# Kernel tuning notes

Measured on AMD Instinct MI355X. Metric: run time of the kernel, lower is better.

## Reference

```python
import jax, jax.numpy as jnp
import numpy as np

B, T, D, H = 64, 512, 512, 512


def setup_inputs() -> dict:
    key = jax.random.key(0)
    k1, k2, k3, k4 = jax.random.split(key, 4)
    return {
        "x": jax.random.normal(k1, (B, T, D), dtype=jnp.float32),
        "kernel": jax.random.normal(k2, (D, 4 * H), dtype=jnp.float32) * 0.02,
        "recurrent_kernel": jax.random.normal(k3, (H, 4 * H), dtype=jnp.float32) * 0.02,
        "bias": jax.random.normal(k4, (4 * H,), dtype=jnp.float32) * 0.02,
    }


def reference(x, kernel, recurrent_kernel, bias):
    # Faithful MyLSTM forward, return_sequences=True.
    # tf.split order along last axis: i, f, c, o.
    b = x.shape[0]
    h0 = jnp.zeros((b, H), dtype=x.dtype)
    c0 = jnp.zeros((b, H), dtype=x.dtype)
    xs = jnp.swapaxes(x, 0, 1)  # [T, B, D]

    def step(carry, xt):
        h, c = carry
        # fused gate GEMM; mathematically identical to the 4 separate matmuls
        z = xt @ kernel + h @ recurrent_kernel + bias  # [B, 4H]
        i_t = jax.nn.sigmoid(z[:, 0 * H:1 * H])
        f_t = jax.nn.sigmoid(z[:, 1 * H:2 * H])
        c_tilde = jnp.tanh(z[:, 2 * H:3 * H])
        o_t = jax.nn.sigmoid(z[:, 3 * H:4 * H])
        # NB: module applies tanh to c_t and carries the ACTIVATED cell state
        c_new = jnp.tanh(f_t * c + i_t * c_tilde)
        h_new = o_t * c_new
        return (h_new, c_new), h_new

    (_, _), hs = jax.lax.scan(step, (h0, c0), xs)
    return jnp.swapaxes(hs, 0, 1)  # [B, T, H]
```

## Files before the change

kernel.cpp:

```cpp
#include <hip/hip_runtime.h>
#include <hip/hip_bf16.h>
#include <stdint.h>


#define Bdim 64
#define Tdim 512
#define Ddim 512
#define Hdim 512
#define G4H  2048
#define NG 4
#define NS 32
#define BH (Bdim * Hdim)

typedef __bf16 bf16_t;
typedef __bf16 bf16x8 __attribute__((ext_vector_type(8)));
typedef float  f32x4  __attribute__((ext_vector_type(4)));
typedef uint32_t u32x4 __attribute__((ext_vector_type(4)));
union pv128 { u32x4 u; f32x4 f; bf16x8 h; };
union bu16 { bf16_t b; unsigned short u; };

__device__ __forceinline__ float sigmoid_f(float x) {
  return 1.0f / (1.0f + __expf(-x));
}
__device__ __forceinline__ float tanh_f(float x) {
  return 1.0f - 2.0f / (__expf(2.0f * x) + 1.0f);
}

__global__ void transpose_bf16_512x2048(const float* __restrict__ src,
                                        bf16_t* __restrict__ dst) {
  __shared__ bf16_t tile[64][72];
  int c0 = blockIdx.x * 64;
  int r0 = blockIdx.y * 64;
  int tx = threadIdx.x & 63;
  int ty = threadIdx.x >> 6;
#pragma unroll
  for (int i = 0; i < 64; i += 4)
    tile[ty + i][tx] = (bf16_t)src[(size_t)(r0 + ty + i) * G4H + c0 + tx];
  __syncthreads();
#pragma unroll
  for (int i = 0; i < 64; i += 4)
    dst[(size_t)(c0 + ty + i) * Ddim + r0 + tx] = tile[tx][ty + i];
}

__global__ void cast_bf16(const float* __restrict__ in, bf16_t* __restrict__ out) {
  size_t i = ((size_t)blockIdx.x * blockDim.x + threadIdx.x) * 8;
  f32x4 a = *(const f32x4*)(in + i);
  f32x4 b = *(const f32x4*)(in + i + 4);
  bf16x8 v;
#pragma unroll
  for (int j = 0; j < 4; ++j) { v[j] = (bf16_t)a[j]; v[j + 4] = (bf16_t)b[j]; }
  *(bf16x8*)(out + i) = v;
}

#define MFMA16(A, B, C) __builtin_amdgcn_mfma_f32_16x16x32_bf16(A, B, C, 0, 0, 0)

#define ISSUE_POLL()                                                         \
  asm volatile(                                                              \
      "global_load_dwordx4 %0, %8, off sc0 sc1\n\t"                          \
      "global_load_dwordx4 %1, %8, off offset:16 sc0 sc1\n\t"                \
      "global_load_dwordx4 %2, %8, off offset:128 sc0 sc1\n\t"               \
      "global_load_dwordx4 %3, %8, off offset:144 sc0 sc1\n\t"               \
      "global_load_dwordx4 %4, %8, off offset:256 sc0 sc1\n\t"               \
      "global_load_dwordx4 %5, %8, off offset:272 sc0 sc1\n\t"               \
      "global_load_dwordx4 %6, %8, off offset:384 sc0 sc1\n\t"               \
      "global_load_dwordx4 %7, %8, off offset:400 sc0 sc1"                   \
      : "=v"(p0.f), "=v"(p1.f), "=v"(p2.f), "=v"(p3.f), "=v"(p4.f),          \
        "=v"(p5.f), "=v"(p6.f), "=v"(p7.f)                                   \
      : "v"(hb)                                                              \
      : "memory")

#define CHECK(P)                                                             \
  do {                                                                       \
    bad |= (P.u[0] ^ st) & 15u;                                              \
    bad |= (P.u[1] ^ st) & 15u;                                              \
    bad |= (P.u[2] ^ st) & 15u;                                              \
    bad |= (P.u[3] ^ st) & 15u;                                              \
  } while (0)

#define HU(PA, PB, c)                                                        \
  do {                                                                       \
    pv128 hi_, lo_;                                                          \
    hi_.u[0] = (PA.u[0] >> 16) | (PA.u[1] & 0xFFFF0000u);                    \
    hi_.u[1] = (PA.u[2] >> 16) | (PA.u[3] & 0xFFFF0000u);                    \
    hi_.u[2] = (PB.u[0] >> 16) | (PB.u[1] & 0xFFFF0000u);                    \
    hi_.u[3] = (PB.u[2] >> 16) | (PB.u[3] & 0xFFFF0000u);                    \
    lo_.u[0] = (PA.u[0] & 0xFFF0u) | ((PA.u[1] & 0xFFF0u) << 16);            \
    lo_.u[1] = (PA.u[2] & 0xFFF0u) | ((PA.u[3] & 0xFFF0u) << 16);            \
    lo_.u[2] = (PB.u[0] & 0xFFF0u) | ((PB.u[1] & 0xFFF0u) << 16);            \
    lo_.u[3] = (PB.u[2] & 0xFFF0u) | ((PB.u[3] & 0xFFF0u) << 16);            \
    a0 = MFMA16(hi_.h, Ur[0][c], a0);                                        \
    a1 = MFMA16(hi_.h, Ur[1][c], a1);                                        \
    a2 = MFMA16(hi_.h, Ur[2][c], a2);                                        \
    a3 = MFMA16(hi_.h, Ur[3][c], a3);                                        \
    a0 = MFMA16(lo_.h, Ur[0][c], a0);                                        \
    a1 = MFMA16(lo_.h, Ur[1][c], a1);                                        \
    a2 = MFMA16(lo_.h, Ur[2][c], a2);                                        \
    a3 = MFMA16(lo_.h, Ur[3][c], a3);                                        \
  } while (0)

__launch_bounds__(256, 1)
__global__ void lstm_fused(const bf16_t* __restrict__ xb,
                           const bf16_t* __restrict__ Wt,
                           const bf16_t* __restrict__ Ut,
                           const float* __restrict__ bias,
                           float* __restrict__ out,
                           uint32_t* __restrict__ hbuf) {
  __shared__ float EX[4][4][16][17];

  const int blk  = blockIdx.x;
  const int g    = blk >> 5;
  const int s    = blk & 31;
  const int wv   = threadIdx.x >> 6;
  const int lane = threadIdx.x & 63;
  const int l15  = lane & 15;
  const int l4   = lane >> 4;
  const int b0   = g * 16;
  const int hc0  = s * 16;
  const int k0   = wv * 128;

  bf16x8 Wr[4][4], Ur[4][4];
#pragma unroll
  for (int G = 0; G < 4; ++G) {
    const bf16_t* wsrc = Wt + (size_t)(G * Hdim + hc0 + l15) * Ddim + k0 + l4 * 8;
    const bf16_t* usrc = Ut + (size_t)(G * Hdim + hc0 + l15) * Ddim + k0 + l4 * 8;
#pragma unroll
    for (int c = 0; c < 4; ++c) {
      Wr[G][c] = *(const bf16x8*)(wsrc + c * 32);
      Ur[G][c] = *(const bf16x8*)(usrc + c * 32);
    }
  }

  const int urow = threadIdx.x >> 4;
  const int ucol = threadIdx.x & 15;
  float b4[4];
#pragma unroll
  for (int G = 0; G < 4; ++G) b4[G] = bias[G * Hdim + hc0 + ucol];
  float cstate = 0.f;
  float* outp = out + (size_t)(b0 + urow) * Tdim * Hdim + hc0 + ucol;
  uint32_t* hpub = hbuf + (size_t)(b0 + urow) * Hdim + hc0 + ucol;
  const uint32_t* hrd = hbuf + (size_t)(b0 + l15) * Hdim + k0 + l4 * 8;
  const bf16_t* xrow = xb + (size_t)(b0 + l15) * Tdim * Ddim + l4 * 8 + k0;

  pv128 xr0, xr1, xr2, xr3;
  asm volatile(
      "global_load_dwordx4 %0, %4, off nt\n\t"
      "global_load_dwordx4 %1, %4, off offset:64 nt\n\t"
      "global_load_dwordx4 %2, %4, off offset:128 nt\n\t"
      "global_load_dwordx4 %3, %4, off offset:192 nt\n\t"
      "s_waitcnt vmcnt(0)"
      : "=v"(xr0.f), "=v"(xr1.f), "=v"(xr2.f), "=v"(xr3.f)
      : "v"(xrow) : "memory");
  __builtin_amdgcn_sched_barrier(0);

  bool dead = false;

  for (int t = 0; t < Tdim; ++t) {
    pv128 p0, p1, p2, p3, p4, p5, p6, p7;
    const uint32_t st = (uint32_t)t & 15u;
    const uint32_t* hb = hrd + (((t - 1) & 1) ? BH : 0);

    if (t > 0 && !dead) {
      ISSUE_POLL();
      __builtin_amdgcn_sched_barrier(0);
    }

    f32x4 a0 = {0, 0, 0, 0}, a1 = {0, 0, 0, 0}, a2 = {0, 0, 0, 0}, a3 = {0, 0, 0, 0};
#define XW(c, xv)                                                            \
    a0 = MFMA16(xv.h, Wr[0][c], a0);                                         \
    a1 = MFMA16(xv.h, Wr[1][c], a1);                                         \
    a2 = MFMA16(xv.h, Wr[2][c], a2);                                         \
    a3 = MFMA16(xv.h, Wr[3][c], a3);
    XW(0, xr0) XW(1, xr1) XW(2, xr2) XW(3, xr3)
#undef XW

    if (t > 0) {
      if (!dead) {
        int guard = 0;
        for (;;) {
          asm volatile("s_waitcnt vmcnt(0)" ::: "memory");
          __builtin_amdgcn_sched_barrier(0);
          uint32_t bad = 0;
          CHECK(p0); CHECK(p1); CHECK(p2); CHECK(p3);
          CHECK(p4); CHECK(p5); CHECK(p6); CHECK(p7);
          if (__all(bad == 0)) break;
          if (++guard > 200000) { dead = true; break; }
          ISSUE_POLL();
          __builtin_amdgcn_sched_barrier(0);
        }
      } else {
        p0.u = p1.u = p2.u = p3.u = p4.u = p5.u = p6.u = p7.u = (u32x4)(0u);
      }
      HU(p0, p1, 0);
      HU(p2, p3, 1);
      HU(p4, p5, 2);
      HU(p6, p7, 3);
    }

    {
      const bf16_t* xp = xrow + (size_t)((t + 1 < Tdim) ? t + 1 : Tdim - 1) * Ddim;
      asm volatile(
          "global_load_dwordx4 %0, %4, off nt\n\t"
          "global_load_dwordx4 %1, %4, off offset:64 nt\n\t"
          "global_load_dwordx4 %2, %4, off offset:128 nt\n\t"
          "global_load_dwordx4 %3, %4, off offset:192 nt"
          : "=v"(xr0.f), "=v"(xr1.f), "=v"(xr2.f), "=v"(xr3.f)
          : "v"(xp) : "memory");
    }

#pragma unroll
    for (int G = 0; G < 4; ++G) {
      f32x4 av = (G == 0) ? a0 : (G == 1) ? a1 : (G == 2) ? a2 : a3;
#pragma unroll
      for (int r = 0; r < 4; ++r) EX[wv][G][l4 * 4 + r][l15] = av[r];
    }
    __syncthreads();

    float z0 = EX[0][0][urow][ucol] + EX[1][0][urow][ucol] +
               EX[2][0][urow][ucol] + EX[3][0][urow][ucol] + b4[0];
    float z1 = EX[0][1][urow][ucol] + EX[1][1][urow][ucol] +
               EX[2][1][urow][ucol] + EX[3][1][urow][ucol] + b4[1];
    float z2 = EX[0][2][urow][ucol] + EX[1][2][urow][ucol] +
               EX[2][2][urow][ucol] + EX[3][2][urow][ucol] + b4[2];
    float z3 = EX[0][3][urow][ucol] + EX[1][3][urow][ucol] +
               EX[2][3][urow][ucol] + EX[3][3][urow][ucol] + b4[3];
    float ig = sigmoid_f(z0), fg = sigmoid_f(z1);
    float ct = tanh_f(z2), og = sigmoid_f(z3);
    float cn = tanh_f(fg * cstate + ig * ct);
    cstate = cn;
    float h = og * cn;

    bu16 hh; hh.b = (bf16_t)h;
    bu16 hl; hl.b = (bf16_t)(h - (float)hh.b);
    uint32_t pubw = ((uint32_t)hh.u << 16) | ((uint32_t)hl.u & 0xFFF0u) |
                    ((uint32_t)(t + 1) & 15u);
    uint32_t* dst = hpub + ((t & 1) ? BH : 0);
    asm volatile("global_store_dword %0, %1, off sc0 sc1" ::"v"(dst), "v"(pubw)
                 : "memory");
    __builtin_nontemporal_store(h, outp + (size_t)t * Hdim);

    __syncthreads();

    asm volatile("s_waitcnt vmcnt(0)" ::: "memory");
    __builtin_amdgcn_sched_barrier(0);
  }
}

extern "C" void kernel_launch(void* const* d_in, const int* in_sizes, int n_in,
                              void* d_out, int out_size, void* d_ws, size_t ws_size,
                              hipStream_t stream) {
  const float* x    = (const float*)d_in[0];
  const float* W    = (const float*)d_in[1];
  const float* U    = (const float*)d_in[2];
  const float* bias = (const float*)d_in[3];
  float* out = (float*)d_out;

  unsigned char* ws = (unsigned char*)d_ws;
  uint32_t* hbuf = (uint32_t*)ws;
  bf16_t* Wt = (bf16_t*)(ws + 262144);
  bf16_t* Ut = Wt + (size_t)G4H * Ddim;
  bf16_t* xb = Ut + (size_t)G4H * Ddim;

  hipMemsetAsync(hbuf, 0, 262144, stream);

  cast_bf16<<<(Bdim * Tdim * Ddim) / 2048, 256, 0, stream>>>(x, xb);

  dim3 tgrid(G4H / 64, Ddim / 64);
  transpose_bf16_512x2048<<<tgrid, 256, 0, stream>>>(W, Wt);
  transpose_bf16_512x2048<<<tgrid, 256, 0, stream>>>(U, Ut);

  lstm_fused<<<NG * NS, 256, 0, stream>>>(xb, Wt, Ut, bias, out, hbuf);
}
```

Measured before the change: 1.526 ms.

## Double-buffer LDS exchange, unroll timestep loop, and relax per-step waits

```diff
diff --git a/kernel.cpp b/kernel.cpp
--- a/kernel.cpp
+++ b/kernel.cpp
@@ -69,25 +69,29 @@
       : "v"(hb)                                                              \
       : "memory")
 
-#define CHECK(P)                                                             \
-  do {                                                                       \
-    bad |= (P.u[0] ^ st) & 15u;                                              \
-    bad |= (P.u[1] ^ st) & 15u;                                              \
-    bad |= (P.u[2] ^ st) & 15u;                                              \
-    bad |= (P.u[3] ^ st) & 15u;                                              \
+#define CHECK8()                                                             \
+  do {                                                                       \
+    bad = (p0.u[0] ^ st) & 15u;                                              \
+    bad |= (p1.u[0] ^ st) & 15u;                                             \
+    bad |= (p2.u[0] ^ st) & 15u;                                             \
+    bad |= (p3.u[0] ^ st) & 15u;                                             \
+    bad |= (p4.u[0] ^ st) & 15u;                                             \
+    bad |= (p5.u[0] ^ st) & 15u;                                             \
+    bad |= (p6.u[0] ^ st) & 15u;                                             \
+    bad |= (p7.u[0] ^ st) & 15u;                                             \
   } while (0)
 
 #define HU(PA, PB, c)                                                        \
   do {                                                                       \
     pv128 hi_, lo_;                                                          \
-    hi_.u[0] = (PA.u[0] >> 16) | (PA.u[1] & 0xFFFF0000u);                    \
-    hi_.u[1] = (PA.u[2] >> 16) | (PA.u[3] & 0xFFFF0000u);                    \
-    hi_.u[2] = (PB.u[0] >> 16) | (PB.u[1] & 0xFFFF0000u);                    \
-    hi_.u[3] = (PB.u[2] >> 16) | (PB.u[3] & 0xFFFF0000u);                    \
-    lo_.u[0] = (PA.u[0] & 0xFFF0u) | ((PA.u[1] & 0xFFF0u) << 16);            \
-    lo_.u[1] = (PA.u[2] & 0xFFF0u) | ((PA.u[3] & 0xFFF0u) << 16);            \
-    lo_.u[2] = (PB.u[0] & 0xFFF0u) | ((PB.u[1] & 0xFFF0u) << 16);            \
-    lo_.u[3] = (PB.u[2] & 0xFFF0u) | ((PB.u[3] & 0xFFF0u) << 16);            \
+    hi_.u[0] = __builtin_amdgcn_perm(PA.u[1], PA.u[0], 0x07060302u);         \
+    hi_.u[1] = __builtin_amdgcn_perm(PA.u[3], PA.u[2], 0x07060302u);         \
+    hi_.u[2] = __builtin_amdgcn_perm(PB.u[1], PB.u[0], 0x07060302u);         \
+    hi_.u[3] = __builtin_amdgcn_perm(PB.u[3], PB.u[2], 0x07060302u);         \
+    lo_.u[0] = __builtin_amdgcn_perm(PA.u[1], PA.u[0], 0x05040100u) & 0xFFF0FFF0u; \
+    lo_.u[1] = __builtin_amdgcn_perm(PA.u[3], PA.u[2], 0x05040100u) & 0xFFF0FFF0u; \
+    lo_.u[2] = __builtin_amdgcn_perm(PB.u[1], PB.u[0], 0x05040100u) & 0xFFF0FFF0u; \
+    lo_.u[3] = __builtin_amdgcn_perm(PB.u[3], PB.u[2], 0x05040100u) & 0xFFF0FFF0u; \
     a0 = MFMA16(hi_.h, Ur[0][c], a0);                                        \
     a1 = MFMA16(hi_.h, Ur[1][c], a1);                                        \
     a2 = MFMA16(hi_.h, Ur[2][c], a2);                                        \
@@ -98,6 +102,97 @@
     a3 = MFMA16(lo_.h, Ur[3][c], a3);                                        \
   } while (0)
 
+#define XW(c, xv)                                                            \
+  a0 = MFMA16(xv.h, Wr[0][c], a0);                                           \
+  a1 = MFMA16(xv.h, Wr[1][c], a1);                                           \
+  a2 = MFMA16(xv.h, Wr[2][c], a2);                                           \
+  a3 = MFMA16(xv.h, Wr[3][c], a3);
+
+#define ISSUE_X(X0, X1, X2, X3, ptr)                                         \
+  asm volatile(                                                              \
+      "global_load_dwordx4 %0, %4, off\n\t"                                  \
+      "global_load_dwordx4 %1, %4, off offset:64\n\t"                        \
+      "global_load_dwordx4 %2, %4, off offset:128\n\t"                       \
+      "global_load_dwordx4 %3, %4, off offset:192"                           \
+      : "=v"(X0.f), "=v"(X1.f), "=v"(X2.f), "=v"(X3.f)                       \
+      : "v"(ptr)                                                             \
+      : "memory")
+
+#define EPILOGUE(T, PAR)                                                     \
+  do {                                                                       \
+    _Pragma("unroll")                                                        \
+    for (int G = 0; G < 4; ++G) {                                            \
+      f32x4 av = (G == 0) ? a0 : (G == 1) ? a1 : (G == 2) ? a2 : a3;         \
+      _Pragma("unroll")                                                      \
+      for (int r = 0; r < 4; ++r) EX[PAR][wv][G][l4 * 4 + r][l15] = av[r];   \
+    }                                                                        \
+    __syncthreads();                                                         \
+    float z0 = EX[PAR][0][0][urow][ucol] + EX[PAR][1][0][urow][ucol] +       \
+               EX[PAR][2][0][urow][ucol] + EX[PAR][3][0][urow][ucol] + b4[0];\
+    float z1 = EX[PAR][0][1][urow][ucol] + EX[PAR][1][1][urow][ucol] +       \
+               EX[PAR][2][1][urow][ucol] + EX[PAR][3][1][urow][ucol] + b4[1];\
+    float z2 = EX[PAR][0][2][urow][ucol] + EX[PAR][1][2][urow][ucol] +       \
+               EX[PAR][2][2][urow][ucol] + EX[PAR][3][2][urow][ucol] + b4[2];\
+    float z3 = EX[PAR][0][3][urow][ucol] + EX[PAR][1][3][urow][ucol] +       \
+               EX[PAR][2][3][urow][ucol] + EX[PAR][3][3][urow][ucol] + b4[3];\
+    float ig = sigmoid_f(z0), fg = sigmoid_f(z1);                            \
+    float ct = tanh_f(z2), og = sigmoid_f(z3);                               \
+    float cn = tanh_f(fg * cstate + ig * ct);                                \
+    cstate = cn;                                                             \
+    float h = og * cn;                                                       \
+    bu16 hh; hh.b = (bf16_t)h;                                               \
+    bu16 hl; hl.b = (bf16_t)(h - (float)hh.b);                               \
+    uint32_t pubw = ((uint32_t)hh.u << 16) | ((uint32_t)hl.u & 0xFFF0u) |    \
+                    ((uint32_t)((T) + 1) & 15u);                             \
+    uint32_t* dstp = hpub + ((PAR) ? BH : 0);                                \
+    asm volatile("global_store_dword %0, %1, off sc0 sc1" ::"v"(dstp),       \
+                 "v"(pubw) : "memory");                                      \
+    float* outw = outp + (size_t)(T) * Hdim;                                 \
+    asm volatile("global_store_dword %0, %1, off nt" ::"v"(outw), "v"(h)     \
+                 : "memory");                                                \
+  } while (0)
+
+#define BODY(T, XU0, XU1, XU2, XU3, XL0, XL1, XL2, XL3, PAR)                 \
+  do {                                                                       \
+    const int t_ = (T);                                                      \
+    asm volatile("s_waitcnt vmcnt(2)" ::: "memory");           \
+    __builtin_amdgcn_sched_barrier(0);                                       \
+    const uint32_t st = (uint32_t)t_ & 15u;                                  \
+    const uint32_t* hb = hrd + ((PAR) ? 0 : BH);          \
+    pv128 p0, p1, p2, p3, p4, p5, p6, p7;                                    \
+    ISSUE_POLL();                                                            \
+    {                                                                        \
+      const bf16_t* xp_ =                                                    \
+          xrow + (size_t)((t_ + 1 < Tdim) ? t_ + 1 : Tdim - 1) * Ddim;       \
+      ISSUE_X(XL0, XL1, XL2, XL3, xp_);                                      \
+    }                                                                        \
+    f32x4 a0 = {0, 0, 0, 0}, a1 = {0, 0, 0, 0};                              \
+    f32x4 a2 = {0, 0, 0, 0}, a3 = {0, 0, 0, 0};                              \
+    XW(0, XU0) XW(1, XU1) XW(2, XU2) XW(3, XU3)                              \
+    {                                                                        \
+      uint32_t bad;                                                          \
+      asm volatile("s_waitcnt vmcnt(4)" ::: "memory");       \
+      __builtin_amdgcn_sched_barrier(0);                                     \
+      CHECK8();                                                              \
+      if (!__all(bad == 0)) {                                                \
+        int guard = 0;                                                       \
+        for (;;) {                                                           \
+          ISSUE_POLL();                                                      \
+          asm volatile("s_waitcnt vmcnt(0)" ::: "memory");                   \
+          __builtin_amdgcn_sched_barrier(0);                                 \
+          CHECK8();                                                          \
+          if (__all(bad == 0)) break;                                        \
+          if (++guard > 200000) break;                                       \
+        }                                                                    \
+      }                                                                      \
+    }                                                                        \
+    HU(p0, p1, 0);                                                           \
+    HU(p2, p3, 1);                                                           \
+    HU(p4, p5, 2);                                                           \
+    HU(p6, p7, 3);                                                           \
+    EPILOGUE(t_, PAR);                                                       \
+  } while (0)
+
 __launch_bounds__(256, 1)
 __global__ void lstm_fused(const bf16_t* __restrict__ xb,
                            const bf16_t* __restrict__ Wt,
@@ -105,7 +200,7 @@
                            const float* __restrict__ bias,
                            float* __restrict__ out,
                            uint32_t* __restrict__ hbuf) {
-  __shared__ float EX[4][4][16][17];
+  __shared__ float EX[2][4][4][16][17];
 
   const int blk  = blockIdx.x;
   const int g    = blk >> 5;
@@ -141,108 +236,24 @@
   const uint32_t* hrd = hbuf + (size_t)(b0 + l15) * Hdim + k0 + l4 * 8;
   const bf16_t* xrow = xb + (size_t)(b0 + l15) * Tdim * Ddim + l4 * 8 + k0;
 
-  pv128 xr0, xr1, xr2, xr3;
-  asm volatile(
-      "global_load_dwordx4 %0, %4, off nt\n\t"
-      "global_load_dwordx4 %1, %4, off offset:64 nt\n\t"
-      "global_load_dwordx4 %2, %4, off offset:128 nt\n\t"
-      "global_load_dwordx4 %3, %4, off offset:192 nt\n\t"
-      "s_waitcnt vmcnt(0)"
-      : "=v"(xr0.f), "=v"(xr1.f), "=v"(xr2.f), "=v"(xr3.f)
-      : "v"(xrow) : "memory");
+  pv128 xA0, xA1, xA2, xA3, xB0, xB1, xB2, xB3;
+
+  ISSUE_X(xA0, xA1, xA2, xA3, xrow);
+  asm volatile("s_waitcnt vmcnt(0)" ::: "memory");
   __builtin_amdgcn_sched_barrier(0);
-
-  bool dead = false;
-
-  for (int t = 0; t < Tdim; ++t) {
-    pv128 p0, p1, p2, p3, p4, p5, p6, p7;
-    const uint32_t st = (uint32_t)t & 15u;
-    const uint32_t* hb = hrd + (((t - 1) & 1) ? BH : 0);
-
-    if (t > 0 && !dead) {
-      ISSUE_POLL();
-      __builtin_amdgcn_sched_barrier(0);
-    }
-
-    f32x4 a0 = {0, 0, 0, 0}, a1 = {0, 0, 0, 0}, a2 = {0, 0, 0, 0}, a3 = {0, 0, 0, 0};
-#define XW(c, xv)                                                            \
-    a0 = MFMA16(xv.h, Wr[0][c], a0);                                         \
-    a1 = MFMA16(xv.h, Wr[1][c], a1);                                         \
-    a2 = MFMA16(xv.h, Wr[2][c], a2);                                         \
-    a3 = MFMA16(xv.h, Wr[3][c], a3);
-    XW(0, xr0) XW(1, xr1) XW(2, xr2) XW(3, xr3)
-#undef XW
-
-    if (t > 0) {
-      if (!dead) {
-        int guard = 0;
-        for (;;) {
-          asm volatile("s_waitcnt vmcnt(0)" ::: "memory");
-          __builtin_amdgcn_sched_barrier(0);
-          uint32_t bad = 0;
-          CHECK(p0); CHECK(p1); CHECK(p2); CHECK(p3);
-          CHECK(p4); CHECK(p5); CHECK(p6); CHECK(p7);
-          if (__all(bad == 0)) break;
-          if (++guard > 200000) { dead = true; break; }
-          ISSUE_POLL();
-          __builtin_amdgcn_sched_barrier(0);
-        }
-      } else {
-        p0.u = p1.u = p2.u = p3.u = p4.u = p5.u = p6.u = p7.u = (u32x4)(0u);
-      }
-      HU(p0, p1, 0);
-      HU(p2, p3, 1);
-      HU(p4, p5, 2);
-      HU(p6, p7, 3);
-    }
-
-    {
-      const bf16_t* xp = xrow + (size_t)((t + 1 < Tdim) ? t + 1 : Tdim - 1) * Ddim;
-      asm volatile(
-          "global_load_dwordx4 %0, %4, off nt\n\t"
-          "global_load_dwordx4 %1, %4, off offset:64 nt\n\t"
-          "global_load_dwordx4 %2, %4, off offset:128 nt\n\t"
-          "global_load_dwordx4 %3, %4, off offset:192 nt"
-          : "=v"(xr0.f), "=v"(xr1.f), "=v"(xr2.f), "=v"(xr3.f)
-          : "v"(xp) : "memory");
-    }
-
-#pragma unroll
-    for (int G = 0; G < 4; ++G) {
-      f32x4 av = (G == 0) ? a0 : (G == 1) ? a1 : (G == 2) ? a2 : a3;
-#pragma unroll
-      for (int r = 0; r < 4; ++r) EX[wv][G][l4 * 4 + r][l15] = av[r];
-    }
-    __syncthreads();
-
-    float z0 = EX[0][0][urow][ucol] + EX[1][0][urow][ucol] +
-               EX[2][0][urow][ucol] + EX[3][0][urow][ucol] + b4[0];
-    float z1 = EX[0][1][urow][ucol] + EX[1][1][urow][ucol] +
-               EX[2][1][urow][ucol] + EX[3][1][urow][ucol] + b4[1];
-    float z2 = EX[0][2][urow][ucol] + EX[1][2][urow][ucol] +
-               EX[2][2][urow][ucol] + EX[3][2][urow][ucol] + b4[2];
-    float z3 = EX[0][3][urow][ucol] + EX[1][3][urow][ucol] +
-               EX[2][3][urow][ucol] + EX[3][3][urow][ucol] + b4[3];
-    float ig = sigmoid_f(z0), fg = sigmoid_f(z1);
-    float ct = tanh_f(z2), og = sigmoid_f(z3);
-    float cn = tanh_f(fg * cstate + ig * ct);
-    cstate = cn;
-    float h = og * cn;
-
-    bu16 hh; hh.b = (bf16_t)h;
-    bu16 hl; hl.b = (bf16_t)(h - (float)hh.b);
-    uint32_t pubw = ((uint32_t)hh.u << 16) | ((uint32_t)hl.u & 0xFFF0u) |
-                    ((uint32_t)(t + 1) & 15u);
-    uint32_t* dst = hpub + ((t & 1) ? BH : 0);
-    asm volatile("global_store_dword %0, %1, off sc0 sc1" ::"v"(dst), "v"(pubw)
-                 : "memory");
-    __builtin_nontemporal_store(h, outp + (size_t)t * Hdim);
-
-    __syncthreads();
-
-    asm volatile("s_waitcnt vmcnt(0)" ::: "memory");
-    __builtin_amdgcn_sched_barrier(0);
+  {
+    ISSUE_X(xB0, xB1, xB2, xB3, xrow + (size_t)Ddim);
+    f32x4 a0 = {0, 0, 0, 0}, a1 = {0, 0, 0, 0};
+    f32x4 a2 = {0, 0, 0, 0}, a3 = {0, 0, 0, 0};
+    XW(0, xA0) XW(1, xA1) XW(2, xA2) XW(3, xA3)
+    EPILOGUE(0, 0);
   }
+
+  for (int t = 1; t < 511; t += 2) {
+    BODY(t,     xB0, xB1, xB2, xB3, xA0, xA1, xA2, xA3, 1);
+    BODY(t + 1, xA0, xA1, xA2, xA3, xB0, xB1, xB2, xB3, 0);
+  }
+  BODY(511, xB0, xB1, xB2, xB3, xA0, xA1, xA2, xA3, 1);
 }
 
 extern "C" void kernel_launch(void* const* d_in, const int* in_sizes, int n_in,
```

Result: slower. 1.952 ms (+27.9%).

## Replace per-element tag polling with per-wave flag polling and double-buffered LDS

Applied to the files above, without the earlier changes.

```diff
diff --git a/kernel.cpp b/kernel.cpp
--- a/kernel.cpp
+++ b/kernel.cpp
@@ -69,25 +69,29 @@
       : "v"(hb)                                                              \
       : "memory")
 
-#define CHECK(P)                                                             \
+#define CHECK8()                                                             \
   do {                                                                       \
-    bad |= (P.u[0] ^ st) & 15u;                                              \
-    bad |= (P.u[1] ^ st) & 15u;                                              \
-    bad |= (P.u[2] ^ st) & 15u;                                              \
-    bad |= (P.u[3] ^ st) & 15u;                                              \
+    bad = (p0.u[0] ^ st) & 15u;                                              \
+    bad |= (p1.u[0] ^ st) & 15u;                                             \
+    bad |= (p2.u[0] ^ st) & 15u;                                             \
+    bad |= (p3.u[0] ^ st) & 15u;                                             \
+    bad |= (p4.u[0] ^ st) & 15u;                                             \
+    bad |= (p5.u[0] ^ st) & 15u;                                             \
+    bad |= (p6.u[0] ^ st) & 15u;                                             \
+    bad |= (p7.u[0] ^ st) & 15u;                                             \
   } while (0)
 
 #define HU(PA, PB, c)                                                        \
   do {                                                                       \
     pv128 hi_, lo_;                                                          \
-    hi_.u[0] = (PA.u[0] >> 16) | (PA.u[1] & 0xFFFF0000u);                    \
-    hi_.u[1] = (PA.u[2] >> 16) | (PA.u[3] & 0xFFFF0000u);                    \
-    hi_.u[2] = (PB.u[0] >> 16) | (PB.u[1] & 0xFFFF0000u);                    \
-    hi_.u[3] = (PB.u[2] >> 16) | (PB.u[3] & 0xFFFF0000u);                    \
-    lo_.u[0] = (PA.u[0] & 0xFFF0u) | ((PA.u[1] & 0xFFF0u) << 16);            \
-    lo_.u[1] = (PA.u[2] & 0xFFF0u) | ((PA.u[3] & 0xFFF0u) << 16);            \
-    lo_.u[2] = (PB.u[0] & 0xFFF0u) | ((PB.u[1] & 0xFFF0u) << 16);            \
-    lo_.u[3] = (PB.u[2] & 0xFFF0u) | ((PB.u[3] & 0xFFF0u) << 16);            \
+    hi_.u[0] = __builtin_amdgcn_perm(PA.u[1], PA.u[0], 0x07060302u);         \
+    hi_.u[1] = __builtin_amdgcn_perm(PA.u[3], PA.u[2], 0x07060302u);         \
+    hi_.u[2] = __builtin_amdgcn_perm(PB.u[1], PB.u[0], 0x07060302u);         \
+    hi_.u[3] = __builtin_amdgcn_perm(PB.u[3], PB.u[2], 0x07060302u);         \
+    lo_.u[0] = __builtin_amdgcn_perm(PA.u[1], PA.u[0], 0x05040100u) & 0xFFF0FFF0u; \
+    lo_.u[1] = __builtin_amdgcn_perm(PA.u[3], PA.u[2], 0x05040100u) & 0xFFF0FFF0u; \
+    lo_.u[2] = __builtin_amdgcn_perm(PB.u[1], PB.u[0], 0x05040100u) & 0xFFF0FFF0u; \
+    lo_.u[3] = __builtin_amdgcn_perm(PB.u[3], PB.u[2], 0x05040100u) & 0xFFF0FFF0u; \
     a0 = MFMA16(hi_.h, Ur[0][c], a0);                                        \
     a1 = MFMA16(hi_.h, Ur[1][c], a1);                                        \
     a2 = MFMA16(hi_.h, Ur[2][c], a2);                                        \
@@ -104,8 +108,9 @@
                            const bf16_t* __restrict__ Ut,
                            const float* __restrict__ bias,
                            float* __restrict__ out,
-                           uint32_t* __restrict__ hbuf) {
-  __shared__ float EX[4][4][16][17];
+                           uint32_t* __restrict__ hbuf,
+                           uint32_t* __restrict__ flags) {
+  __shared__ float EX[2][4][4][16][17];
 
   const int blk  = blockIdx.x;
   const int g    = blk >> 5;
@@ -141,6 +146,10 @@
   const uint32_t* hrd = hbuf + (size_t)(b0 + l15) * Hdim + k0 + l4 * 8;
   const bf16_t* xrow = xb + (size_t)(b0 + l15) * Tdim * Ddim + l4 * 8 + k0;
 
+  uint32_t* fpub = flags + ((size_t)(g * NS + s) * 4 + wv) * 16;
+  const uint32_t* fpoll =
+      flags + ((size_t)(g * NS + wv * 8 + ((lane >> 2) & 7)) * 4 + (lane & 3)) * 16;
+
   pv128 xr0, xr1, xr2, xr3;
   asm volatile(
       "global_load_dwordx4 %0, %4, off nt\n\t"
@@ -152,14 +161,12 @@
       : "v"(xrow) : "memory");
   __builtin_amdgcn_sched_barrier(0);
 
-  bool dead = false;
-
   for (int t = 0; t < Tdim; ++t) {
     pv128 p0, p1, p2, p3, p4, p5, p6, p7;
     const uint32_t st = (uint32_t)t & 15u;
     const uint32_t* hb = hrd + (((t - 1) & 1) ? BH : 0);
 
-    if (t > 0 && !dead) {
+    if (t > 0) {
       ISSUE_POLL();
       __builtin_amdgcn_sched_barrier(0);
     }
@@ -174,21 +181,28 @@
 #undef XW
 
     if (t > 0) {
-      if (!dead) {
+      uint32_t bad;
+      asm volatile("s_waitcnt vmcnt(0)" ::: "memory");
+      __builtin_amdgcn_sched_barrier(0);
+      CHECK8();
+      if (!__all(bad == 0)) {
         int guard = 0;
         for (;;) {
+          uint32_t fv;
+          asm volatile("global_load_dword %0, %1, off sc0 sc1\n\t"
+                       "s_waitcnt vmcnt(0)"
+                       : "=v"(fv) : "v"(fpoll) : "memory");
+          if (__all((int)(fv >= (uint32_t)t))) break;
+          if (++guard > 500000) break;
+        }
+        for (;;) {
+          ISSUE_POLL();
           asm volatile("s_waitcnt vmcnt(0)" ::: "memory");
           __builtin_amdgcn_sched_barrier(0);
-          uint32_t bad = 0;
-          CHECK(p0); CHECK(p1); CHECK(p2); CHECK(p3);
-          CHECK(p4); CHECK(p5); CHECK(p6); CHECK(p7);
+          CHECK8();
           if (__all(bad == 0)) break;
-          if (++guard > 200000) { dead = true; break; }
-          ISSUE_POLL();
-          __builtin_amdgcn_sched_barrier(0);
+          if (++guard > 500000) break;
         }
-      } else {
-        p0.u = p1.u = p2.u = p3.u = p4.u = p5.u = p6.u = p7.u = (u32x4)(0u);
       }
       HU(p0, p1, 0);
       HU(p2, p3, 1);
@@ -207,22 +221,23 @@
           : "v"(xp) : "memory");
     }
 
+    const int par = t & 1;
 #pragma unroll
     for (int G = 0; G < 4; ++G) {
       f32x4 av = (G == 0) ? a0 : (G == 1) ? a1 : (G == 2) ? a2 : a3;
 #pragma unroll
-      for (int r = 0; r < 4; ++r) EX[wv][G][l4 * 4 + r][l15] = av[r];
+      for (int r = 0; r < 4; ++r) EX[par][wv][G][l4 * 4 + r][l15] = av[r];
     }
     __syncthreads();
 
-    float z0 = EX[0][0][urow][ucol] + EX[1][0][urow][ucol] +
-               EX[2][0][urow][ucol] + EX[3][0][urow][ucol] + b4[0];
-    float z1 = EX[0][1][urow][ucol] + EX[1][1][urow][ucol] +
-               EX[2][1][urow][ucol] + EX[3][1][urow][ucol] + b4[1];
-    float z2 = EX[0][2][urow][ucol] + EX[1][2][urow][ucol] +
-               EX[2][2][urow][ucol] + EX[3][2][urow][ucol] + b4[2];
-    float z3 = EX[0][3][urow][ucol] + EX[1][3][urow][ucol] +
-               EX[2][3][urow][ucol] + EX[3][3][urow][ucol] + b4[3];
+    float z0 = EX[par][0][0][urow][ucol] + EX[par][1][0][urow][ucol] +
+               EX[par][2][0][urow][ucol] + EX[par][3][0][urow][ucol] + b4[0];
+    float z1 = EX[par][0][1][urow][ucol] + EX[par][1][1][urow][ucol] +
+               EX[par][2][1][urow][ucol] + EX[par][3][1][urow][ucol] + b4[1];
+    float z2 = EX[par][0][2][urow][ucol] + EX[par][1][2][urow][ucol] +
+               EX[par][2][2][urow][ucol] + EX[par][3][2][urow][ucol] + b4[2];
+    float z3 = EX[par][0][3][urow][ucol] + EX[par][1][3][urow][ucol] +
+               EX[par][2][3][urow][ucol] + EX[par][3][3][urow][ucol] + b4[3];
     float ig = sigmoid_f(z0), fg = sigmoid_f(z1);
     float ct = tanh_f(z2), og = sigmoid_f(z3);
     float cn = tanh_f(fg * cstate + ig * ct);
@@ -233,12 +248,16 @@
     bu16 hl; hl.b = (bf16_t)(h - (float)hh.b);
     uint32_t pubw = ((uint32_t)hh.u << 16) | ((uint32_t)hl.u & 0xFFF0u) |
                     ((uint32_t)(t + 1) & 15u);
-    uint32_t* dst = hpub + ((t & 1) ? BH : 0);
+    uint32_t* dst = hpub + (par ? BH : 0);
     asm volatile("global_store_dword %0, %1, off sc0 sc1" ::"v"(dst), "v"(pubw)
                  : "memory");
     __builtin_nontemporal_store(h, outp + (size_t)t * Hdim);
 
-    __syncthreads();
+    if (lane == 0) {
+      uint32_t stamp = (uint32_t)(t + 1);
+      asm volatile("global_store_dword %0, %1, off sc0 sc1" ::"v"(fpub),
+                   "v"(stamp) : "memory");
+    }
 
     asm volatile("s_waitcnt vmcnt(0)" ::: "memory");
     __builtin_amdgcn_sched_barrier(0);
@@ -255,12 +274,13 @@
   float* out = (float*)d_out;
 
   unsigned char* ws = (unsigned char*)d_ws;
-  uint32_t* hbuf = (uint32_t*)ws;
-  bf16_t* Wt = (bf16_t*)(ws + 262144);
+  uint32_t* flags = (uint32_t*)ws;
+  uint32_t* hbuf  = (uint32_t*)(ws + 32768);
+  bf16_t* Wt = (bf16_t*)(ws + 32768 + 262144);
   bf16_t* Ut = Wt + (size_t)G4H * Ddim;
   bf16_t* xb = Ut + (size_t)G4H * Ddim;
 
-  hipMemsetAsync(hbuf, 0, 262144, stream);
+  hipMemsetAsync(ws, 0, 32768 + 262144, stream);
 
   cast_bf16<<<(Bdim * Tdim * Ddim) / 2048, 256, 0, stream>>>(x, xb);
 
@@ -268,5 +288,5 @@
   transpose_bf16_512x2048<<<tgrid, 256, 0, stream>>>(W, Wt);
   transpose_bf16_512x2048<<<tgrid, 256, 0, stream>>>(U, Ut);
 
-  lstm_fused<<<NG * NS, 256, 0, stream>>>(xb, Wt, Ut, bias, out, hbuf);
-}
+  lstm_fused<<<NG * NS, 256, 0, stream>>>(xb, Wt, Ut, bias, out, hbuf, flags);
+}
```

After: 1.824 ms. +19.6%, slower.
